# Optimization experiments

Hardware: AMD Instinct MI355X
Metric: run time of the kernel (lower is better)

Reference implementation:

```python
import jax, jax.numpy as jnp
import numpy as np

C = 256
DQK = C // 8


def setup_inputs() -> dict:
    key = jax.random.key(0)
    ks = jax.random.split(key, 7)
    B, H, W = 8, 64, 64
    x = jax.random.normal(ks[0], (B, H, W, C), dtype=jnp.float32)
    # 1x1 conv weights (equivalent to per-pixel dense): [Cin, Cout] + bias
    sq = 1.0 / np.sqrt(C)
    Wq = jax.random.normal(ks[1], (C, DQK), dtype=jnp.float32) * sq
    bq = jnp.zeros((DQK,), dtype=jnp.float32)
    Wk = jax.random.normal(ks[2], (C, DQK), dtype=jnp.float32) * sq
    bk = jnp.zeros((DQK,), dtype=jnp.float32)
    Wv = jax.random.normal(ks[3], (C, C), dtype=jnp.float32) * sq
    bv = jnp.zeros((C,), dtype=jnp.float32)
    gamma = jnp.float32(0.5)  # nonzero so attention path affects output/grads
    return {"x": x, "Wq": Wq, "bq": bq, "Wk": Wk, "bk": bk,
            "Wv": Wv, "bv": bv, "gamma": gamma}


def reference(x, Wq, bq, Wk, bk, Wv, bv, gamma):
    B, H, W, c = x.shape
    n = H * W
    xf = x.reshape(B, n, c)                      # [B, hw, C]
    q = xf @ Wq + bq                              # [B, hw, C//8]
    k = xf @ Wk + bk                              # [B, hw, C//8]
    v = xf @ Wv + bv                              # [B, hw, C]
    scores = jnp.einsum('bnd,bmd->bnm', q, k)     # [B, hw, hw], no scaling (faithful)
    attn = jax.nn.softmax(scores, axis=-1)
    out = jnp.einsum('bnm,bmc->bnc', attn, v)     # [B, hw, C]
    out = out.reshape(B, H, W, c)
    return gamma * out + x
```

## Files before the change

kernel.cpp:

```cpp
#include <hip/hip_runtime.h>
#include <hip/hip_bf16.h>
#include <math.h>

#define B_ 8
#define N_ 4096
#define C_ 256
#define DQK_ 32

typedef float f32x4  __attribute__((ext_vector_type(4)));
typedef float f32x16 __attribute__((ext_vector_type(16)));
typedef short bf16x8 __attribute__((ext_vector_type(8)));
typedef short bf16x4 __attribute__((ext_vector_type(4)));

__device__ __forceinline__ short f2bf(float f){
  union { float f; unsigned u; } v; v.f = f;
  unsigned r = v.u + 0x7fffu + ((v.u >> 16) & 1u);
  return (short)(r >> 16);
}

__global__ void cast_wt_kernel(const float* __restrict__ Wq, const float* __restrict__ Wk,
                               const float* __restrict__ Wv, short* __restrict__ WT){
  int n = blockIdx.x;
  int k = threadIdx.x;
  float val;
  if (n < 32)       val = Wq[k*32 + n];
  else if (n < 64)  val = Wk[k*32 + (n-32)];
  else              val = Wv[k*256 + (n-64)];
  WT[n*256 + k] = f2bf(val);
}

__global__ __launch_bounds__(256) void proj_kernel(
    const float* __restrict__ x, const short* __restrict__ WT,
    const float* __restrict__ bq, const float* __restrict__ bk, const float* __restrict__ bv,
    short* __restrict__ qws, short* __restrict__ kws, short* __restrict__ vSw){
  __shared__ __align__(16) short sX[64*264];
  __shared__ __align__(16) short sT[64*72];
  int tid = threadIdx.x;
  int lane = tid & 63, wave = tid >> 6;
  int lane15 = lane & 15, quad = lane >> 4;
  int mbase = blockIdx.x * 64;
  int b = mbase >> 12, kvb = mbase & (N_-1);

  const float* xr = x + (size_t)mbase * C_;
  for (int i = 0; i < 8; i++){
    int s = tid + i*256;
    int row = s >> 5, cg = (s & 31) << 3;
    const f32x4* src = (const f32x4*)(xr + row*C_ + cg);
    f32x4 a = src[0], c = src[1];
    bf16x8 p;
    p[0]=f2bf(a[0]); p[1]=f2bf(a[1]); p[2]=f2bf(a[2]); p[3]=f2bf(a[3]);
    p[4]=f2bf(c[0]); p[5]=f2bf(c[1]); p[6]=f2bf(c[2]); p[7]=f2bf(c[3]);
    *(bf16x8*)(sX + row*264 + cg) = p;
  }
  __syncthreads();

  f32x4 acc[5][4];
  for (int i=0;i<5;i++) for (int mt=0;mt<4;mt++) acc[i][mt] = (f32x4)(0.f);

  for (int kc = 0; kc < 8; kc++){
    bf16x8 afr[4];
    #pragma unroll
    for (int mt=0;mt<4;mt++)
      afr[mt] = *(const bf16x8*)(sX + (mt*16+lane15)*264 + kc*32 + quad*8);
    bf16x8 bfr[5];
    #pragma unroll
    for (int i=0;i<5;i++){
      int t = i*4 + wave;
      bfr[i] = *(const bf16x8*)(WT + (size_t)(t*16+lane15)*256 + kc*32 + quad*8);
    }
    #pragma unroll
    for (int i=0;i<5;i++)
      #pragma unroll
      for (int mt=0;mt<4;mt++)
        acc[i][mt] = __builtin_amdgcn_mfma_f32_16x16x32_bf16(afr[mt], bfr[i], acc[i][mt], 0,0,0);
  }

  #pragma unroll
  for (int i=0;i<5;i++){
    int t = i*4 + wave;
    int n0 = t*16 + lane15;
    float bias = (n0 < 32) ? bq[n0] : (n0 < 64 ? bk[n0-32] : bv[n0-64]);
    if (n0 < 64){
      #pragma unroll
      for (int mt=0;mt<4;mt++)
        #pragma unroll
        for (int r=0;r<4;r++)
          sT[(mt*16 + quad*4 + r)*72 + n0] = f2bf(acc[i][mt][r] + bias);
    } else {
      int ch = n0 - 64, cht = ch >> 5, c5 = ch & 31;
      int lanep = c5 | ((quad & 1) << 5);
      int jo = (quad >> 1) * 4;
      #pragma unroll
      for (int mt=0;mt<4;mt++){
        bf16x4 pk;
        pk[0]=f2bf(acc[i][mt][0]+bias); pk[1]=f2bf(acc[i][mt][1]+bias);
        pk[2]=f2bf(acc[i][mt][2]+bias); pk[3]=f2bf(acc[i][mt][3]+bias);
        size_t off = (size_t)b*1048576 + (size_t)(kvb>>6)*16384
                   + (size_t)(mt*8 + cht)*512 + (size_t)lanep*8 + jo;
        *(bf16x4*)(vSw + off) = pk;
      }
    }
  }
  __syncthreads();

  {
    int qt = tid >> 7, p = (tid >> 6) & 1, ln = tid & 63;
    int row = qt*32 + (ln & 31);
    int dcol = p*16 + (ln >> 5)*8;
    bf16x8 vq = *(const bf16x8*)(sT + row*72 + dcol);
    bf16x8 vk = *(const bf16x8*)(sT + row*72 + 32 + dcol);
    size_t qoff = ((((size_t)b*128 + ((kvb>>5) + qt))*2 + p)*64 + ln)*8;
    *(bf16x8*)(qws + qoff) = vq;
    size_t koff = ((size_t)b*64 + (kvb>>6))*2048 + (size_t)((qt*2 + p)*64 + ln)*8;
    *(bf16x8*)(kws + koff) = vk;
  }
}

__global__ __launch_bounds__(512, 2) void flash_kernel(
    const float* __restrict__ x, const short* __restrict__ qws, const short* __restrict__ kws,
    const short* __restrict__ vSw, const float* __restrict__ gptr, float* __restrict__ out){
  __shared__ __align__(16) char smem[66560];
  short* sV0 = (short*)smem;
  short* sV1 = (short*)(smem + 32768);
  int tid = threadIdx.x;
  int lane = tid & 63, wave = tid >> 6;
  int l31 = lane & 31, h = lane >> 5;
  int qt = wave >> 1, kh = wave & 1;
  int b = blockIdx.x & 7;
  int q0 = (blockIdx.x >> 3) << 7;

  const short* qb = qws + (size_t)b*131072;
  const short* kb = kws + (size_t)b*131072;
  const short* vb = vSw + (size_t)b*1048576;

  int qtg = (q0 >> 5) + qt;
  bf16x8 qf0 = *(const bf16x8*)(qb + (size_t)((qtg*2+0)*64 + lane)*8);
  bf16x8 qf1 = *(const bf16x8*)(qb + (size_t)((qtg*2+1)*64 + lane)*8);

  const short* kf0p = kb + (size_t)((2*kh+0)*64 + lane)*8;
  const short* kf1p = kb + (size_t)((2*kh+1)*64 + lane)*8;
  bf16x8 kA0 = *(const bf16x8*)(kf0p);
  bf16x8 kA1 = *(const bf16x8*)(kf1p);
  bf16x8 kB0 = *(const bf16x8*)(kf0p + 2048);
  bf16x8 kB1 = *(const bf16x8*)(kf1p + 2048);

#define VPREF(CHUNK, DST) do { \
    const short* vsrc_ = vb + (size_t)(CHUNK)*16384; \
    _Pragma("unroll") \
    for (int r_=0;r_<4;r_++) \
      __builtin_amdgcn_global_load_lds( \
        (const __attribute__((address_space(1))) void*)(vsrc_ + (size_t)(r_*512+tid)*8), \
        (__attribute__((address_space(3))) void*)((DST) + (size_t)(r_*512+tid)*8), 16, 0, 0); \
  } while(0)

#define QKS(K0, K1) ({ \
    f32x16 t_ = __builtin_amdgcn_mfma_f32_32x32x16_bf16((K0), qf0, (f32x16)(0.f), 0,0,0); \
    __builtin_amdgcn_mfma_f32_32x32x16_bf16((K1), qf1, t_, 0,0,0); })

#define EXPPACK(S, PF) do { \
    float ls_ = 0.f; \
    _Pragma("unroll") \
    for (int g_=0; g_<2; g_++){ \
      union { bf16x8 v; unsigned u[4]; } P_; \
      _Pragma("unroll") \
      for (int j_=0;j_<4;j_++){ \
        float2 e_; \
        e_.x = __expf((S)[g_*8 + 2*j_]); \
        e_.y = __expf((S)[g_*8 + 2*j_ + 1]); \
        ls_ += e_.x + e_.y; \
        __hip_bfloat162 t2_ = __float22bfloat162_rn(e_); \
        __builtin_memcpy(&P_.u[j_], &t2_, 4); \
      } \
      (PF)[g_] = P_.v; \
    } \
    rsum += ls_; \
  } while(0)

#define PV_STEP(SVC, PF) do { \
    _Pragma("unroll") \
    for (int g_=0; g_<2; g_++){ \
      const short* base_ = (SVC) + (2*kh + g_)*4096; \
      _Pragma("unroll") \
      for (int cht_=0; cht_<8; cht_++){ \
        bf16x8 vf_ = *(const bf16x8*)(base_ + (cht_*64 + lane)*8); \
        acc[cht_] = __builtin_amdgcn_mfma_f32_32x32x16_bf16((PF)[g_], vf_, acc[cht_], 0,0,0); \
      } \
    } \
  } while(0)

  VPREF(0, sV0);
  __syncthreads();

  f32x16 acc[8];
  #pragma unroll
  for (int t=0;t<8;t++) acc[t] = (f32x16)(0.f);
  float rsum = 0.f;

  f32x16 s0 = QKS(kA0, kA1);
  f32x16 s1 = (f32x16)(0.f);
  kA0 = *(const bf16x8*)(kf0p + 2*2048);
  kA1 = *(const bf16x8*)(kf1p + 2*2048);

  for (int it2 = 0; it2 < 32; it2++){
    {
      VPREF(2*it2+1, sV1);
      bf16x8 pf[2];
      EXPPACK(s0, pf);
      s1 = QKS(kB0, kB1);
      if (it2 < 31){
        kB0 = *(const bf16x8*)(kf0p + (size_t)(2*it2+3)*2048);
        kB1 = *(const bf16x8*)(kf1p + (size_t)(2*it2+3)*2048);
      }
      PV_STEP(sV0, pf);
      __syncthreads();
    }
    {
      if (it2 < 31) VPREF(2*it2+2, sV0);
      bf16x8 pf[2];
      EXPPACK(s1, pf);
      if (it2 < 31){
        s0 = QKS(kA0, kA1);
        if (it2 < 30){
          kA0 = *(const bf16x8*)(kf0p + (size_t)(2*it2+4)*2048);
          kA1 = *(const bf16x8*)(kf1p + (size_t)(2*it2+4)*2048);
        }
      }
      PV_STEP(sV1, pf);
      __syncthreads();
    }
  }

  float* R1 = (float*)smem;
  float* TAB = (float*)(smem + 65536);
  int pw = wave ^ 1;
  rsum += __shfl_xor(rsum, 32);
  if (lane < 32) TAB[wave*32 + lane] = rsum;

  if (kh == 0){
    #pragma unroll
    for (int i=0;i<16;i++){ R1[wave*2048 + i*64 + lane] = acc[4][i];
                            R1[wave*2048 + 1024 + i*64 + lane] = acc[5][i]; }
  } else {
    #pragma unroll
    for (int i=0;i<16;i++){ R1[wave*2048 + i*64 + lane] = acc[0][i];
                            R1[wave*2048 + 1024 + i*64 + lane] = acc[1][i]; }
  }
  __syncthreads();
  if (kh == 0){
    #pragma unroll
    for (int i=0;i<16;i++){ acc[0][i] += R1[pw*2048 + i*64 + lane];
                            acc[1][i] += R1[pw*2048 + 1024 + i*64 + lane]; }
  } else {
    #pragma unroll
    for (int i=0;i<16;i++){ acc[4][i] += R1[pw*2048 + i*64 + lane];
                            acc[5][i] += R1[pw*2048 + 1024 + i*64 + lane]; }
  }
  __syncthreads();
  if (kh == 0){
    #pragma unroll
    for (int i=0;i<16;i++){ R1[wave*2048 + i*64 + lane] = acc[6][i];
                            R1[wave*2048 + 1024 + i*64 + lane] = acc[7][i]; }
  } else {
    #pragma unroll
    for (int i=0;i<16;i++){ R1[wave*2048 + i*64 + lane] = acc[2][i];
                            R1[wave*2048 + 1024 + i*64 + lane] = acc[3][i]; }
  }
  __syncthreads();
  if (kh == 0){
    #pragma unroll
    for (int i=0;i<16;i++){ acc[2][i] += R1[pw*2048 + i*64 + lane];
                            acc[3][i] += R1[pw*2048 + 1024 + i*64 + lane]; }
  } else {
    #pragma unroll
    for (int i=0;i<16;i++){ acc[6][i] += R1[pw*2048 + i*64 + lane];
                            acc[7][i] += R1[pw*2048 + 1024 + i*64 + lane]; }
  }

  float g = *gptr;
  const float* xb = x + ((size_t)b*N_ + q0 + qt*32)*C_;
  float*       ob = out + ((size_t)b*N_ + q0 + qt*32)*C_;
  if (kh == 0){
    #pragma unroll
    for (int i=0;i<16;i++){
      int q = (i&3) + 8*(i>>2) + 4*h;
      float rv = 1.f / (TAB[(qt*2+0)*32 + q] + TAB[(qt*2+1)*32 + q]);
      #pragma unroll
      for (int ct=0; ct<4; ct++){
        int ch = ct*32 + l31;
        ob[(size_t)q*C_ + ch] = g*(acc[ct][i]*rv) + xb[(size_t)q*C_ + ch];
      }
    }
  } else {
    #pragma unroll
    for (int i=0;i<16;i++){
      int q = (i&3) + 8*(i>>2) + 4*h;
      float rv = 1.f / (TAB[(qt*2+0)*32 + q] + TAB[(qt*2+1)*32 + q]);
      #pragma unroll
      for (int ct=0; ct<4; ct++){
        int ch = (4+ct)*32 + l31;
        ob[(size_t)q*C_ + ch] = g*(acc[4+ct][i]*rv) + xb[(size_t)q*C_ + ch];
      }
    }
  }
#undef VPREF
#undef QKS
#undef EXPPACK
#undef PV_STEP
}

extern "C" void kernel_launch(void* const* d_in, const int* in_sizes, int n_in,
                              void* d_out, int out_size, void* d_ws, size_t ws_size,
                              hipStream_t stream){
  const float* x  = (const float*)d_in[0];
  const float* Wq = (const float*)d_in[1];
  const float* bq = (const float*)d_in[2];
  const float* Wk = (const float*)d_in[3];
  const float* bk = (const float*)d_in[4];
  const float* Wv = (const float*)d_in[5];
  const float* bv = (const float*)d_in[6];
  const float* gm = (const float*)d_in[7];
  float* out = (float*)d_out;
  char* ws = (char*)d_ws;
  short* WT  = (short*)ws;
  short* qws = (short*)(ws + 163840);
  short* kws = (short*)(ws + 163840 + 2097152);
  short* vSw = (short*)(ws + 163840 + 2*2097152);

  cast_wt_kernel<<<dim3(320), dim3(256), 0, stream>>>(Wq, Wk, Wv, WT);
  proj_kernel<<<dim3(512), dim3(256), 0, stream>>>(x, WT, bq, bk, bv, qws, kws, vSw);
  flash_kernel<<<dim3(256), dim3(512), 0, stream>>>(x, qws, kws, vSw, gm, out);
}
```

Baseline: 191.6 us.

## Process two query tiles per wave to reuse V fragments across MFMAs

Halves the block to 4 waves, each computing two 32-row query tiles so every V fragment read from LDS feeds two MFMAs, and lets each wave own a full output tile after the cross-wave reduction. This is meant to cut LDS read traffic per MFMA and wave count overhead. It doubles accumulator register use and forces one block per CU, lowering occupancy and latency hiding.

```diff
diff --git a/kernel.cpp b/kernel.cpp
--- a/kernel.cpp
+++ b/kernel.cpp
@@ -116,16 +116,16 @@
   }
 }
 
-__global__ __launch_bounds__(512, 2) void flash_kernel(
+__global__ __launch_bounds__(256, 1) void flash_kernel(
     const float* __restrict__ x, const short* __restrict__ qws, const short* __restrict__ kws,
     const short* __restrict__ vSw, const float* __restrict__ gptr, float* __restrict__ out){
-  __shared__ __align__(16) char smem[66560];
+  __shared__ __align__(16) char smem[67072];
   short* sV0 = (short*)smem;
   short* sV1 = (short*)(smem + 32768);
   int tid = threadIdx.x;
   int lane = tid & 63, wave = tid >> 6;
   int l31 = lane & 31, h = lane >> 5;
-  int qt = wave >> 1, kh = wave & 1;
+  int qtp = wave >> 1, kh = wave & 1;
   int b = blockIdx.x & 7;
   int q0 = (blockIdx.x >> 3) << 7;
 
@@ -133,31 +133,29 @@
   const short* kb = kws + (size_t)b*131072;
   const short* vb = vSw + (size_t)b*1048576;
 
-  int qtg = (q0 >> 5) + qt;
-  bf16x8 qf0 = *(const bf16x8*)(qb + (size_t)((qtg*2+0)*64 + lane)*8);
-  bf16x8 qf1 = *(const bf16x8*)(qb + (size_t)((qtg*2+1)*64 + lane)*8);
+  int qtgA = (q0 >> 5) + qtp*2;
+  bf16x8 qfA0 = *(const bf16x8*)(qb + (size_t)((qtgA*2+0)*64 + lane)*8);
+  bf16x8 qfA1 = *(const bf16x8*)(qb + (size_t)((qtgA*2+1)*64 + lane)*8);
+  bf16x8 qfB0 = *(const bf16x8*)(qb + (size_t)(((qtgA+1)*2+0)*64 + lane)*8);
+  bf16x8 qfB1 = *(const bf16x8*)(qb + (size_t)(((qtgA+1)*2+1)*64 + lane)*8);
 
   const short* kf0p = kb + (size_t)((2*kh+0)*64 + lane)*8;
   const short* kf1p = kb + (size_t)((2*kh+1)*64 + lane)*8;
-  bf16x8 kA0 = *(const bf16x8*)(kf0p);
-  bf16x8 kA1 = *(const bf16x8*)(kf1p);
-  bf16x8 kB0 = *(const bf16x8*)(kf0p + 2048);
-  bf16x8 kB1 = *(const bf16x8*)(kf1p + 2048);
+  bf16x8 kE0 = *(const bf16x8*)(kf0p);
+  bf16x8 kE1 = *(const bf16x8*)(kf1p);
+  bf16x8 kO0 = *(const bf16x8*)(kf0p + 2048);
+  bf16x8 kO1 = *(const bf16x8*)(kf1p + 2048);
 
 #define VPREF(CHUNK, DST) do { \
     const short* vsrc_ = vb + (size_t)(CHUNK)*16384; \
     _Pragma("unroll") \
-    for (int r_=0;r_<4;r_++) \
+    for (int r_=0;r_<8;r_++) \
       __builtin_amdgcn_global_load_lds( \
-        (const __attribute__((address_space(1))) void*)(vsrc_ + (size_t)(r_*512+tid)*8), \
-        (__attribute__((address_space(3))) void*)((DST) + (size_t)(r_*512+tid)*8), 16, 0, 0); \
+        (const __attribute__((address_space(1))) void*)(vsrc_ + (size_t)(r_*256+tid)*8), \
+        (__attribute__((address_space(3))) void*)((DST) + (size_t)(r_*256+tid)*8), 16, 0, 0); \
   } while(0)
 
-#define QKS(K0, K1) ({ \
-    f32x16 t_ = __builtin_amdgcn_mfma_f32_32x32x16_bf16((K0), qf0, (f32x16)(0.f), 0,0,0); \
-    __builtin_amdgcn_mfma_f32_32x32x16_bf16((K1), qf1, t_, 0,0,0); })
-
-#define EXPPACK(S, PF) do { \
+#define EXPPACK(S, PF, RS) do { \
     float ls_ = 0.f; \
     _Pragma("unroll") \
     for (int g_=0; g_<2; g_++){ \
@@ -173,139 +171,169 @@
       } \
       (PF)[g_] = P_.v; \
     } \
-    rsum += ls_; \
+    (RS) += ls_; \
   } while(0)
 
-#define PV_STEP(SVC, PF) do { \
+#define QK2(K0, K1, NFA, NFB) do { \
+    f32x16 sA_ = __builtin_amdgcn_mfma_f32_32x32x16_bf16((K0), qfA0, (f32x16)(0.f), 0,0,0); \
+    sA_        = __builtin_amdgcn_mfma_f32_32x32x16_bf16((K1), qfA1, sA_, 0,0,0); \
+    f32x16 sB_ = __builtin_amdgcn_mfma_f32_32x32x16_bf16((K0), qfB0, (f32x16)(0.f), 0,0,0); \
+    sB_        = __builtin_amdgcn_mfma_f32_32x32x16_bf16((K1), qfB1, sB_, 0,0,0); \
+    EXPPACK(sA_, NFA, rsA); \
+    EXPPACK(sB_, NFB, rsB); \
+  } while(0)
+
+#define PV2(SVC) do { \
     _Pragma("unroll") \
-    for (int g_=0; g_<2; g_++){ \
-      const short* base_ = (SVC) + (2*kh + g_)*4096; \
+    for (int ks_=0; ks_<2; ks_++){ \
+      const short* base_ = (SVC) + (2*kh + ks_)*4096; \
       _Pragma("unroll") \
       for (int cht_=0; cht_<8; cht_++){ \
-        bf16x8 vf_ = *(const bf16x8*)(base_ + (cht_*64 + lane)*8); \
-        acc[cht_] = __builtin_amdgcn_mfma_f32_32x32x16_bf16((PF)[g_], vf_, acc[cht_], 0,0,0); \
+        bf16x8 vf_ = *(const bf16x8*)(base_ + cht_*512 + lane*8); \
+        accA[cht_] = __builtin_amdgcn_mfma_f32_32x32x16_bf16(pfA[ks_], vf_, accA[cht_], 0,0,0); \
+        accB[cht_] = __builtin_amdgcn_mfma_f32_32x32x16_bf16(pfB[ks_], vf_, accB[cht_], 0,0,0); \
       } \
     } \
   } while(0)
 
   VPREF(0, sV0);
-  __syncthreads();
-
-  f32x16 acc[8];
+
+  f32x16 accA[8], accB[8];
   #pragma unroll
-  for (int t=0;t<8;t++) acc[t] = (f32x16)(0.f);
-  float rsum = 0.f;
-
-  f32x16 s0 = QKS(kA0, kA1);
-  f32x16 s1 = (f32x16)(0.f);
-  kA0 = *(const bf16x8*)(kf0p + 2*2048);
-  kA1 = *(const bf16x8*)(kf1p + 2*2048);
-
-  for (int it2 = 0; it2 < 32; it2++){
+  for (int t=0;t<8;t++){ accA[t] = (f32x16)(0.f); accB[t] = (f32x16)(0.f); }
+  float rsA = 0.f, rsB = 0.f;
+  bf16x8 pfA[2], pfB[2];
+
+  QK2(kE0, kE1, pfA, pfB);
+  kE0 = *(const bf16x8*)(kf0p + 2*2048);
+  kE1 = *(const bf16x8*)(kf1p + 2*2048);
+  __syncthreads();
+
+  for (int j = 0; j < 32; j++){
     {
-      VPREF(2*it2+1, sV1);
-      bf16x8 pf[2];
-      EXPPACK(s0, pf);
-      s1 = QKS(kB0, kB1);
-      if (it2 < 31){
-        kB0 = *(const bf16x8*)(kf0p + (size_t)(2*it2+3)*2048);
-        kB1 = *(const bf16x8*)(kf1p + (size_t)(2*it2+3)*2048);
-      }
-      PV_STEP(sV0, pf);
+      VPREF(2*j+1, sV1);
+      bf16x8 nfA[2], nfB[2];
+      QK2(kO0, kO1, nfA, nfB);
+      if (j < 31){
+        kO0 = *(const bf16x8*)(kf0p + (size_t)(2*j+3)*2048);
+        kO1 = *(const bf16x8*)(kf1p + (size_t)(2*j+3)*2048);
+      }
+      PV2(sV0);
+      pfA[0]=nfA[0]; pfA[1]=nfA[1]; pfB[0]=nfB[0]; pfB[1]=nfB[1];
       __syncthreads();
     }
     {
-      if (it2 < 31) VPREF(2*it2+2, sV0);
-      bf16x8 pf[2];
-      EXPPACK(s1, pf);
-      if (it2 < 31){
-        s0 = QKS(kA0, kA1);
-        if (it2 < 30){
-          kA0 = *(const bf16x8*)(kf0p + (size_t)(2*it2+4)*2048);
-          kA1 = *(const bf16x8*)(kf1p + (size_t)(2*it2+4)*2048);
+      if (j < 31){
+        VPREF(2*j+2, sV0);
+        bf16x8 nfA[2], nfB[2];
+        QK2(kE0, kE1, nfA, nfB);
+        if (j < 30){
+          kE0 = *(const bf16x8*)(kf0p + (size_t)(2*j+4)*2048);
+          kE1 = *(const bf16x8*)(kf1p + (size_t)(2*j+4)*2048);
         }
-      }
-      PV_STEP(sV1, pf);
+        PV2(sV1);
+        pfA[0]=nfA[0]; pfA[1]=nfA[1]; pfB[0]=nfB[0]; pfB[1]=nfB[1];
+      } else {
+        PV2(sV1);
+      }
       __syncthreads();
     }
   }
 
-  float* R1 = (float*)smem;
-  float* TAB = (float*)(smem + 65536);
+  rsA += __shfl_xor(rsA, 32);
+  rsB += __shfl_xor(rsB, 32);
+
+  float* R   = (float*)smem;
+  float* RS  = (float*)(smem + 65536);
+  float* RSM = (float*)(smem + 66560);
   int pw = wave ^ 1;
-  rsum += __shfl_xor(rsum, 32);
-  if (lane < 32) TAB[wave*32 + lane] = rsum;
+  if (lane < 32){ RS[wave*64 + l31] = rsA; RS[wave*64 + 32 + l31] = rsB; }
 
   if (kh == 0){
     #pragma unroll
-    for (int i=0;i<16;i++){ R1[wave*2048 + i*64 + lane] = acc[4][i];
-                            R1[wave*2048 + 1024 + i*64 + lane] = acc[5][i]; }
+    for (int c=0;c<4;c++)
+      #pragma unroll
+      for (int i=0;i<16;i++) R[wave*4096 + c*1024 + i*64 + lane] = accB[c][i];
   } else {
     #pragma unroll
-    for (int i=0;i<16;i++){ R1[wave*2048 + i*64 + lane] = acc[0][i];
-                            R1[wave*2048 + 1024 + i*64 + lane] = acc[1][i]; }
+    for (int c=0;c<4;c++)
+      #pragma unroll
+      for (int i=0;i<16;i++) R[wave*4096 + c*1024 + i*64 + lane] = accA[c][i];
+  }
+  __syncthreads();
+  {
+    float rsT;
+    if (kh == 0){
+      #pragma unroll
+      for (int c=0;c<4;c++)
+        #pragma unroll
+        for (int i=0;i<16;i++) accA[c][i] += R[pw*4096 + c*1024 + i*64 + lane];
+      rsT = rsA + RS[pw*64 + l31];
+    } else {
+      #pragma unroll
+      for (int c=0;c<4;c++)
+        #pragma unroll
+        for (int i=0;i<16;i++) accB[c][i] += R[pw*4096 + c*1024 + i*64 + lane];
+      rsT = rsB + RS[pw*64 + 32 + l31];
+    }
+    if (lane < 32) RSM[wave*32 + l31] = rsT;
   }
   __syncthreads();
   if (kh == 0){
     #pragma unroll
-    for (int i=0;i<16;i++){ acc[0][i] += R1[pw*2048 + i*64 + lane];
-                            acc[1][i] += R1[pw*2048 + 1024 + i*64 + lane]; }
+    for (int c=0;c<4;c++)
+      #pragma unroll
+      for (int i=0;i<16;i++) R[wave*4096 + c*1024 + i*64 + lane] = accB[4+c][i];
   } else {
     #pragma unroll
-    for (int i=0;i<16;i++){ acc[4][i] += R1[pw*2048 + i*64 + lane];
-                            acc[5][i] += R1[pw*2048 + 1024 + i*64 + lane]; }
+    for (int c=0;c<4;c++)
+      #pragma unroll
+      for (int i=0;i<16;i++) R[wave*4096 + c*1024 + i*64 + lane] = accA[4+c][i];
   }
   __syncthreads();
   if (kh == 0){
     #pragma unroll
-    for (int i=0;i<16;i++){ R1[wave*2048 + i*64 + lane] = acc[6][i];
-                            R1[wave*2048 + 1024 + i*64 + lane] = acc[7][i]; }
+    for (int c=0;c<4;c++)
+      #pragma unroll
+      for (int i=0;i<16;i++) accA[4+c][i] += R[pw*4096 + c*1024 + i*64 + lane];
   } else {
     #pragma unroll
-    for (int i=0;i<16;i++){ R1[wave*2048 + i*64 + lane] = acc[2][i];
-                            R1[wave*2048 + 1024 + i*64 + lane] = acc[3][i]; }
-  }
-  __syncthreads();
-  if (kh == 0){
-    #pragma unroll
-    for (int i=0;i<16;i++){ acc[2][i] += R1[pw*2048 + i*64 + lane];
-                            acc[3][i] += R1[pw*2048 + 1024 + i*64 + lane]; }
-  } else {
-    #pragma unroll
-    for (int i=0;i<16;i++){ acc[6][i] += R1[pw*2048 + i*64 + lane];
-                            acc[7][i] += R1[pw*2048 + 1024 + i*64 + lane]; }
+    for (int c=0;c<4;c++)
+      #pragma unroll
+      for (int i=0;i<16;i++) accB[4+c][i] += R[pw*4096 + c*1024 + i*64 + lane];
   }
 
   float g = *gptr;
-  const float* xb = x + ((size_t)b*N_ + q0 + qt*32)*C_;
-  float*       ob = out + ((size_t)b*N_ + q0 + qt*32)*C_;
+  int kt = qtp*2 + kh;
+  const float* xb = x + ((size_t)b*N_ + q0 + kt*32)*C_;
+  float*       ob = out + ((size_t)b*N_ + q0 + kt*32)*C_;
   if (kh == 0){
     #pragma unroll
     for (int i=0;i<16;i++){
       int q = (i&3) + 8*(i>>2) + 4*h;
-      float rv = 1.f / (TAB[(qt*2+0)*32 + q] + TAB[(qt*2+1)*32 + q]);
-      #pragma unroll
-      for (int ct=0; ct<4; ct++){
-        int ch = ct*32 + l31;
-        ob[(size_t)q*C_ + ch] = g*(acc[ct][i]*rv) + xb[(size_t)q*C_ + ch];
+      float rv = 1.f / RSM[wave*32 + q];
+      #pragma unroll
+      for (int c=0;c<8;c++){
+        int ch = c*32 + l31;
+        ob[(size_t)q*C_ + ch] = g*(accA[c][i]*rv) + xb[(size_t)q*C_ + ch];
       }
     }
   } else {
     #pragma unroll
     for (int i=0;i<16;i++){
       int q = (i&3) + 8*(i>>2) + 4*h;
-      float rv = 1.f / (TAB[(qt*2+0)*32 + q] + TAB[(qt*2+1)*32 + q]);
-      #pragma unroll
-      for (int ct=0; ct<4; ct++){
-        int ch = (4+ct)*32 + l31;
-        ob[(size_t)q*C_ + ch] = g*(acc[4+ct][i]*rv) + xb[(size_t)q*C_ + ch];
+      float rv = 1.f / RSM[wave*32 + q];
+      #pragma unroll
+      for (int c=0;c<8;c++){
+        int ch = c*32 + l31;
+        ob[(size_t)q*C_ + ch] = g*(accB[c][i]*rv) + xb[(size_t)q*C_ + ch];
       }
     }
   }
 #undef VPREF
-#undef QKS
 #undef EXPPACK
-#undef PV_STEP
+#undef QK2
+#undef PV2
 }
 
 extern "C" void kernel_launch(void* const* d_in, const int* in_sizes, int n_in,
@@ -328,5 +356,5 @@
 
   cast_wt_kernel<<<dim3(320), dim3(256), 0, stream>>>(Wq, Wk, Wv, WT);
   proj_kernel<<<dim3(512), dim3(256), 0, stream>>>(x, WT, bq, bk, bv, qws, kws, vSw);
-  flash_kernel<<<dim3(256), dim3(512), 0, stream>>>(x, qws, kws, vSw, gm, out);
-}
+  flash_kernel<<<dim3(256), dim3(256), 0, stream>>>(x, qws, kws, vSw, gm, out);
+}
```

Measured after the change: 262.9 us. 37.2% more time.

## Remap waves to two query tiles and half the channels for V-fragment reuse

Applied to the files above, without the earlier changes.

Each wave now computes scores for two 32-row query tiles (A and B) against its key half, then accumulates PV for only half of the 256 channels. Every V fragment loaded from LDS feeds two MFMAs, which halves LDS reads per MFMA. The cost is that the QK^T and exp work is duplicated across the two channel-half waves. The old two-stage software pipeline of score computation is also replaced by a simpler single loop, so there is less overlap between the score MFMAs and the PV MFMAs.

```diff
diff --git a/kernel.cpp b/kernel.cpp
--- a/kernel.cpp
+++ b/kernel.cpp
@@ -119,13 +119,13 @@
 __global__ __launch_bounds__(512, 2) void flash_kernel(
     const float* __restrict__ x, const short* __restrict__ qws, const short* __restrict__ kws,
     const short* __restrict__ vSw, const float* __restrict__ gptr, float* __restrict__ out){
-  __shared__ __align__(16) char smem[66560];
+  __shared__ __align__(16) char smem[67584];
   short* sV0 = (short*)smem;
   short* sV1 = (short*)(smem + 32768);
   int tid = threadIdx.x;
   int lane = tid & 63, wave = tid >> 6;
   int l31 = lane & 31, h = lane >> 5;
-  int qt = wave >> 1, kh = wave & 1;
+  int qp = wave >> 2, cd = (wave >> 1) & 1, kh = wave & 1;
   int b = blockIdx.x & 7;
   int q0 = (blockIdx.x >> 3) << 7;
 
@@ -133,16 +133,16 @@
   const short* kb = kws + (size_t)b*131072;
   const short* vb = vSw + (size_t)b*1048576;
 
-  int qtg = (q0 >> 5) + qt;
-  bf16x8 qf0 = *(const bf16x8*)(qb + (size_t)((qtg*2+0)*64 + lane)*8);
-  bf16x8 qf1 = *(const bf16x8*)(qb + (size_t)((qtg*2+1)*64 + lane)*8);
+  int qtgA = (q0 >> 5) + qp*2;
+  bf16x8 qfA0 = *(const bf16x8*)(qb + (size_t)((qtgA*2+0)*64 + lane)*8);
+  bf16x8 qfA1 = *(const bf16x8*)(qb + (size_t)((qtgA*2+1)*64 + lane)*8);
+  bf16x8 qfB0 = *(const bf16x8*)(qb + (size_t)(((qtgA+1)*2+0)*64 + lane)*8);
+  bf16x8 qfB1 = *(const bf16x8*)(qb + (size_t)(((qtgA+1)*2+1)*64 + lane)*8);
 
   const short* kf0p = kb + (size_t)((2*kh+0)*64 + lane)*8;
   const short* kf1p = kb + (size_t)((2*kh+1)*64 + lane)*8;
-  bf16x8 kA0 = *(const bf16x8*)(kf0p);
-  bf16x8 kA1 = *(const bf16x8*)(kf1p);
-  bf16x8 kB0 = *(const bf16x8*)(kf0p + 2048);
-  bf16x8 kB1 = *(const bf16x8*)(kf1p + 2048);
+  bf16x8 kfc0 = *(const bf16x8*)(kf0p);
+  bf16x8 kfc1 = *(const bf16x8*)(kf1p);
 
 #define VPREF(CHUNK, DST) do { \
     const short* vsrc_ = vb + (size_t)(CHUNK)*16384; \
@@ -153,11 +153,7 @@
         (__attribute__((address_space(3))) void*)((DST) + (size_t)(r_*512+tid)*8), 16, 0, 0); \
   } while(0)
 
-#define QKS(K0, K1) ({ \
-    f32x16 t_ = __builtin_amdgcn_mfma_f32_32x32x16_bf16((K0), qf0, (f32x16)(0.f), 0,0,0); \
-    __builtin_amdgcn_mfma_f32_32x32x16_bf16((K1), qf1, t_, 0,0,0); })
-
-#define EXPPACK(S, PF) do { \
+#define EXPPACK(S, PF, RS) do { \
     float ls_ = 0.f; \
     _Pragma("unroll") \
     for (int g_=0; g_<2; g_++){ \
@@ -173,139 +169,129 @@
       } \
       (PF)[g_] = P_.v; \
     } \
-    rsum += ls_; \
+    (RS) += ls_; \
   } while(0)
 
-#define PV_STEP(SVC, PF) do { \
-    _Pragma("unroll") \
-    for (int g_=0; g_<2; g_++){ \
-      const short* base_ = (SVC) + (2*kh + g_)*4096; \
-      _Pragma("unroll") \
-      for (int cht_=0; cht_<8; cht_++){ \
-        bf16x8 vf_ = *(const bf16x8*)(base_ + (cht_*64 + lane)*8); \
-        acc[cht_] = __builtin_amdgcn_mfma_f32_32x32x16_bf16((PF)[g_], vf_, acc[cht_], 0,0,0); \
-      } \
-    } \
-  } while(0)
-
   VPREF(0, sV0);
   __syncthreads();
 
-  f32x16 acc[8];
+  f32x16 accA[4], accB[4];
   #pragma unroll
-  for (int t=0;t<8;t++) acc[t] = (f32x16)(0.f);
-  float rsum = 0.f;
-
-  f32x16 s0 = QKS(kA0, kA1);
-  f32x16 s1 = (f32x16)(0.f);
-  kA0 = *(const bf16x8*)(kf0p + 2*2048);
-  kA1 = *(const bf16x8*)(kf1p + 2*2048);
-
-  for (int it2 = 0; it2 < 32; it2++){
+  for (int t=0;t<4;t++){ accA[t] = (f32x16)(0.f); accB[t] = (f32x16)(0.f); }
+  float rsA = 0.f, rsB = 0.f;
+
+  for (int it=0; it<64; it++){
+    short* sVc = (it & 1) ? sV1 : sV0;
+    short* sVn = (it & 1) ? sV0 : sV1;
+    if (it < 63) VPREF(it+1, sVn);
+
+    bf16x8 pfA[2], pfB[2];
     {
-      VPREF(2*it2+1, sV1);
-      bf16x8 pf[2];
-      EXPPACK(s0, pf);
-      s1 = QKS(kB0, kB1);
-      if (it2 < 31){
-        kB0 = *(const bf16x8*)(kf0p + (size_t)(2*it2+3)*2048);
-        kB1 = *(const bf16x8*)(kf1p + (size_t)(2*it2+3)*2048);
+      f32x16 s = __builtin_amdgcn_mfma_f32_32x32x16_bf16(kfc0, qfA0, (f32x16)(0.f), 0,0,0);
+      s        = __builtin_amdgcn_mfma_f32_32x32x16_bf16(kfc1, qfA1, s, 0,0,0);
+      EXPPACK(s, pfA, rsA);
+    }
+    {
+      f32x16 s = __builtin_amdgcn_mfma_f32_32x32x16_bf16(kfc0, qfB0, (f32x16)(0.f), 0,0,0);
+      s        = __builtin_amdgcn_mfma_f32_32x32x16_bf16(kfc1, qfB1, s, 0,0,0);
+      EXPPACK(s, pfB, rsB);
+    }
+    if (it < 63){
+      kfc0 = *(const bf16x8*)(kf0p + (size_t)(it+1)*2048);
+      kfc1 = *(const bf16x8*)(kf1p + (size_t)(it+1)*2048);
+    }
+
+    #pragma unroll
+    for (int ks=0; ks<2; ks++){
+      const short* base = sVc + (2*kh + ks)*4096;
+      #pragma unroll
+      for (int c=0; c<4; c++){
+        bf16x8 vf = *(const bf16x8*)(base + ((cd*4+c)*64 + lane)*8);
+        accA[c] = __builtin_amdgcn_mfma_f32_32x32x16_bf16(pfA[ks], vf, accA[c], 0,0,0);
+        accB[c] = __builtin_amdgcn_mfma_f32_32x32x16_bf16(pfB[ks], vf, accB[c], 0,0,0);
       }
-      PV_STEP(sV0, pf);
-      __syncthreads();
-    }
-    {
-      if (it2 < 31) VPREF(2*it2+2, sV0);
-      bf16x8 pf[2];
-      EXPPACK(s1, pf);
-      if (it2 < 31){
-        s0 = QKS(kA0, kA1);
-        if (it2 < 30){
-          kA0 = *(const bf16x8*)(kf0p + (size_t)(2*it2+4)*2048);
-          kA1 = *(const bf16x8*)(kf1p + (size_t)(2*it2+4)*2048);
-        }
-      }
-      PV_STEP(sV1, pf);
-      __syncthreads();
-    }
-  }
-
-  float* R1 = (float*)smem;
-  float* TAB = (float*)(smem + 65536);
+    }
+    __syncthreads();
+  }
+
+  rsA += __shfl_xor(rsA, 32);
+  rsB += __shfl_xor(rsB, 32);
+  float* R  = (float*)smem;
+  float* RS = (float*)(smem + 65536);
   int pw = wave ^ 1;
-  rsum += __shfl_xor(rsum, 32);
-  if (lane < 32) TAB[wave*32 + lane] = rsum;
-
-  if (kh == 0){
-    #pragma unroll
-    for (int i=0;i<16;i++){ R1[wave*2048 + i*64 + lane] = acc[4][i];
-                            R1[wave*2048 + 1024 + i*64 + lane] = acc[5][i]; }
-  } else {
-    #pragma unroll
-    for (int i=0;i<16;i++){ R1[wave*2048 + i*64 + lane] = acc[0][i];
-                            R1[wave*2048 + 1024 + i*64 + lane] = acc[1][i]; }
-  }
-  __syncthreads();
-  if (kh == 0){
-    #pragma unroll
-    for (int i=0;i<16;i++){ acc[0][i] += R1[pw*2048 + i*64 + lane];
-                            acc[1][i] += R1[pw*2048 + 1024 + i*64 + lane]; }
-  } else {
-    #pragma unroll
-    for (int i=0;i<16;i++){ acc[4][i] += R1[pw*2048 + i*64 + lane];
-                            acc[5][i] += R1[pw*2048 + 1024 + i*64 + lane]; }
-  }
-  __syncthreads();
-  if (kh == 0){
-    #pragma unroll
-    for (int i=0;i<16;i++){ R1[wave*2048 + i*64 + lane] = acc[6][i];
-                            R1[wave*2048 + 1024 + i*64 + lane] = acc[7][i]; }
-  } else {
-    #pragma unroll
-    for (int i=0;i<16;i++){ R1[wave*2048 + i*64 + lane] = acc[2][i];
-                            R1[wave*2048 + 1024 + i*64 + lane] = acc[3][i]; }
-  }
-  __syncthreads();
-  if (kh == 0){
-    #pragma unroll
-    for (int i=0;i<16;i++){ acc[2][i] += R1[pw*2048 + i*64 + lane];
-                            acc[3][i] += R1[pw*2048 + 1024 + i*64 + lane]; }
-  } else {
-    #pragma unroll
-    for (int i=0;i<16;i++){ acc[6][i] += R1[pw*2048 + i*64 + lane];
-                            acc[7][i] += R1[pw*2048 + 1024 + i*64 + lane]; }
+  if (cd == 0 && lane < 32){ RS[wave*64 + l31] = rsA; RS[wave*64 + 32 + l31] = rsB; }
+
+  if (kh == 0){
+    #pragma unroll
+    for (int i=0;i<16;i++){ R[wave*2048 + i*64 + lane] = accB[0][i];
+                            R[wave*2048 + 1024 + i*64 + lane] = accB[1][i]; }
+  } else {
+    #pragma unroll
+    for (int i=0;i<16;i++){ R[wave*2048 + i*64 + lane] = accA[0][i];
+                            R[wave*2048 + 1024 + i*64 + lane] = accA[1][i]; }
+  }
+  __syncthreads();
+  if (kh == 0){
+    #pragma unroll
+    for (int i=0;i<16;i++){ accA[0][i] += R[pw*2048 + i*64 + lane];
+                            accA[1][i] += R[pw*2048 + 1024 + i*64 + lane]; }
+  } else {
+    #pragma unroll
+    for (int i=0;i<16;i++){ accB[0][i] += R[pw*2048 + i*64 + lane];
+                            accB[1][i] += R[pw*2048 + 1024 + i*64 + lane]; }
+  }
+  __syncthreads();
+  if (kh == 0){
+    #pragma unroll
+    for (int i=0;i<16;i++){ R[wave*2048 + i*64 + lane] = accB[2][i];
+                            R[wave*2048 + 1024 + i*64 + lane] = accB[3][i]; }
+  } else {
+    #pragma unroll
+    for (int i=0;i<16;i++){ R[wave*2048 + i*64 + lane] = accA[2][i];
+                            R[wave*2048 + 1024 + i*64 + lane] = accA[3][i]; }
+  }
+  __syncthreads();
+  if (kh == 0){
+    #pragma unroll
+    for (int i=0;i<16;i++){ accA[2][i] += R[pw*2048 + i*64 + lane];
+                            accA[3][i] += R[pw*2048 + 1024 + i*64 + lane]; }
+  } else {
+    #pragma unroll
+    for (int i=0;i<16;i++){ accB[2][i] += R[pw*2048 + i*64 + lane];
+                            accB[3][i] += R[pw*2048 + 1024 + i*64 + lane]; }
   }
 
   float g = *gptr;
-  const float* xb = x + ((size_t)b*N_ + q0 + qt*32)*C_;
-  float*       ob = out + ((size_t)b*N_ + q0 + qt*32)*C_;
+  int kt = qp*2 + kh;
+  int w0 = qp*4, w1 = qp*4 + 1;
+  int sel = kh*32;
+  const float* xb = x + ((size_t)b*N_ + q0 + kt*32)*C_;
+  float*       ob = out + ((size_t)b*N_ + q0 + kt*32)*C_;
   if (kh == 0){
     #pragma unroll
     for (int i=0;i<16;i++){
       int q = (i&3) + 8*(i>>2) + 4*h;
-      float rv = 1.f / (TAB[(qt*2+0)*32 + q] + TAB[(qt*2+1)*32 + q]);
-      #pragma unroll
-      for (int ct=0; ct<4; ct++){
-        int ch = ct*32 + l31;
-        ob[(size_t)q*C_ + ch] = g*(acc[ct][i]*rv) + xb[(size_t)q*C_ + ch];
+      float rv = 1.f / (RS[w0*64 + sel + q] + RS[w1*64 + sel + q]);
+      #pragma unroll
+      for (int c=0;c<4;c++){
+        int ch = (cd*4 + c)*32 + l31;
+        ob[(size_t)q*C_ + ch] = g*(accA[c][i]*rv) + xb[(size_t)q*C_ + ch];
       }
     }
   } else {
     #pragma unroll
     for (int i=0;i<16;i++){
       int q = (i&3) + 8*(i>>2) + 4*h;
-      float rv = 1.f / (TAB[(qt*2+0)*32 + q] + TAB[(qt*2+1)*32 + q]);
-      #pragma unroll
-      for (int ct=0; ct<4; ct++){
-        int ch = (4+ct)*32 + l31;
-        ob[(size_t)q*C_ + ch] = g*(acc[4+ct][i]*rv) + xb[(size_t)q*C_ + ch];
+      float rv = 1.f / (RS[w0*64 + sel + q] + RS[w1*64 + sel + q]);
+      #pragma unroll
+      for (int c=0;c<4;c++){
+        int ch = (cd*4 + c)*32 + l31;
+        ob[(size_t)q*C_ + ch] = g*(accB[c][i]*rv) + xb[(size_t)q*C_ + ch];
       }
     }
   }
 #undef VPREF
-#undef QKS
 #undef EXPPACK
-#undef PV_STEP
 }
 
 extern "C" void kernel_launch(void* const* d_in, const int* in_sizes, int n_in,
```

Result: slower. 197.9 us (+3.3%).
